# Optimization experiments

Hardware: AMD Instinct MI355X
Metric: run time of the kernel (lower is better)

## Reference

```python
import jax, jax.numpy as jnp
import numpy as np

INPUT_DIM, ATTN_DIM, OUTPUT_DIM = 1024, 1024, 1024
B, LQ, LKV = 4, 2048, 2048


def setup_inputs() -> dict:
    key = jax.random.key(0)
    ks = jax.random.split(key, 10)
    s = 1.0 / np.sqrt(INPUT_DIM)
    return {
        "primary": jax.random.normal(ks[0], (B, LQ, INPUT_DIM), jnp.float32),
        "context_sequence": jax.random.normal(ks[1], (B, LKV, INPUT_DIM), jnp.float32),
        "mask": jax.random.randint(ks[2], (B, LQ, LKV), 0, 2).astype(jnp.float32),
        "Wq": jax.random.uniform(ks[3], (INPUT_DIM, ATTN_DIM), jnp.float32, -s, s),
        "bq": jax.random.uniform(ks[4], (ATTN_DIM,), jnp.float32, -s, s),
        "Wk": jax.random.uniform(ks[5], (INPUT_DIM, ATTN_DIM), jnp.float32, -s, s),
        "bk": jax.random.uniform(ks[6], (ATTN_DIM,), jnp.float32, -s, s),
        "Wv": jax.random.uniform(ks[7], (INPUT_DIM, OUTPUT_DIM), jnp.float32, -s, s),
        "bv": jax.random.uniform(ks[8], (OUTPUT_DIM,), jnp.float32, -s, s),
    }


def reference(primary, context_sequence, mask, Wq, bq, Wk, bk, Wv, bv):
    q = primary @ Wq + bq                      # [B, Lq, attn_dim]
    k = context_sequence @ Wk + bk             # [B, Lkv, attn_dim]
    v = context_sequence @ Wv + bv             # [B, Lkv, output_dim]
    score = jnp.einsum('bqd,bkd->bqk', q, k) / jnp.sqrt(jnp.float32(ATTN_DIM))
    score = score + mask * (-1e9)
    attn = jax.nn.softmax(score, axis=-1)
    return jnp.einsum('bqk,bkd->bqd', attn, v)  # [B, Lq, output_dim]
```

## Files before the change

kernel.cpp:

```cpp
#include <hip/hip_runtime.h>
#include <stdint.h>

typedef unsigned short u16;
typedef unsigned char u8;
typedef __bf16 bf16_t;
typedef bf16_t bf16x8 __attribute__((ext_vector_type(8)));
typedef float f32x4 __attribute__((ext_vector_type(4)));
typedef u16 u16x4 __attribute__((ext_vector_type(4)));
typedef u16 u16x8 __attribute__((ext_vector_type(8)));

__device__ __forceinline__ u16 f2bf(float f) {
  union { float f; uint32_t u; } v;
  v.f = f;
  uint32_t u = v.u + 0x7fffu + ((v.u >> 16) & 1u);
  return (u16)(u >> 16);
}

__device__ __forceinline__ float bf2f(u16 x) {
  union { uint32_t u; float f; } v;
  v.u = ((uint32_t)x) << 16;
  return v.f;
}

__device__ __forceinline__ void gload16(const void* g, void* l) {
  __builtin_amdgcn_global_load_lds(
      (__attribute__((address_space(1))) void*)g,
      (__attribute__((address_space(3))) void*)l, 16, 0, 0);
}

__device__ __forceinline__ f32x4 mfma16(bf16x8 a, bf16x8 b, f32x4 c) {
  return __builtin_amdgcn_mfma_f32_16x16x32_bf16(a, b, c, 0, 0, 0);
}

__global__ __launch_bounds__(256) void cvt_wt(
    const float* __restrict__ prim, u16* __restrict__ prim_bf,
    const float* __restrict__ ctx, u16* __restrict__ ctx_bf,
    const float* __restrict__ Wq, const float* __restrict__ Wk,
    const float* __restrict__ Wv, u16* __restrict__ Oq,
    u16* __restrict__ Ok, u16* __restrict__ Ov) {
  int b = blockIdx.x;
  if (b < 2048) {
    const float* in = (b < 1024) ? prim : ctx;
    u16* out = (b < 1024) ? prim_bf : ctx_bf;
    int bb = b & 1023;
    int i = bb * 256 + threadIdx.x;
    const int n4 = 2097152;
    for (; i < n4; i += 1024 * 256) {
      float4 v = *((const float4*)in + i);
      u16x4 o;
      o.x = f2bf(v.x); o.y = f2bf(v.y); o.z = f2bf(v.z); o.w = f2bf(v.w);
      *((u16x4*)out + i) = o;
    }
  } else {
    int tb = b - 2048;
    int zi = tb >> 10, rem = tb & 1023;
    const float* W = zi == 0 ? Wq : (zi == 1 ? Wk : Wv);
    u16* O = zi == 0 ? Oq : (zi == 1 ? Ok : Ov);
    __shared__ float t[32][33];
    int x = threadIdx.x & 31, y = threadIdx.x >> 5;
    int n0 = (rem & 31) * 32, k0 = (rem >> 5) * 32;
#pragma unroll
    for (int i = 0; i < 32; i += 8)
      t[y + i][x] = W[(size_t)(k0 + y + i) * 1024 + n0 + x];
    __syncthreads();
#pragma unroll
    for (int i = 0; i < 32; i += 8)
      O[(size_t)(n0 + y + i) * 1024 + k0 + x] = f2bf(t[x][y + i]);
  }
}

template <typename CT>
__device__ __forceinline__ void gemm_body(
    u16* aL, u16* bL,
    const u16* __restrict__ A, const u16* __restrict__ Bt,
    const float* __restrict__ biasCol, const float* __restrict__ biasRow,
    CT* __restrict__ C, int bm, int bn, int K, int lda, int ldb, int ldc) {
  int tid = threadIdx.x;
  int lane = tid & 63, w = tid >> 6;
  int l15 = lane & 15, g = lane >> 4;
  int wr = w >> 2, wc = w & 3;
  int NT = K >> 6;

  f32x4 acc[8][4] = {};

  auto stageA = [&](int buf, int h, int tk) {
    int k0 = tk * 64;
    int r = tid >> 3, cd = (tid & 7) * 8;
    int cs = cd ^ ((r & 7) * 8);
    int row0 = h * 64 + r;
    gload16(A + (size_t)(bm + row0) * lda + k0 + cs, aL + buf * 16384 + row0 * 64 + cd);
    int row1 = row0 + 128;
    gload16(A + (size_t)(bm + row1) * lda + k0 + cs, aL + buf * 16384 + row1 * 64 + cd);
  };
  auto stageB = [&](int buf, int x, int tk) {
    int k0 = tk * 64;
#pragma unroll
    for (int l = 0; l < 2; ++l) {
      int u = l * 512 + tid;
      int r = u >> 3, cd = (u & 7) * 8;
      int cs = cd ^ ((r & 7) * 8);
      int row = x * 128 + r;
      gload16(Bt + (size_t)(bn + row) * ldb + k0 + cs, bL + buf * 16384 + row * 64 + cd);
    }
  };
  auto ldA = [&](int buf, int m, int kc) -> bf16x8 {
    int row = wr * 128 + m * 16 + l15;
    int col = (kc * 32 + g * 8) ^ ((row & 7) * 8);
    return *(const bf16x8*)(aL + buf * 16384 + row * 64 + col);
  };
  auto ldB = [&](int buf, int j, int kc) -> bf16x8 {
    int row = wc * 64 + j * 16 + l15;
    int col = (kc * 32 + g * 8) ^ ((row & 7) * 8);
    return *(const bf16x8*)(bL + buf * 16384 + row * 64 + col);
  };

  stageA(0, 0, 0);
  stageB(0, 0, 0);
  stageB(0, 1, 0);
  stageA(0, 1, 0);
  int t1c = NT > 1 ? 1 : 0;
  stageA(1, 0, t1c);
  stageB(1, 0, t1c);
  asm volatile("s_waitcnt vmcnt(6)" ::: "memory");
  __builtin_amdgcn_s_barrier();

  for (int t = 0; t < NT; ++t) {
    int cur = t & 1, nxt = cur ^ 1;
    int tn1 = (t + 1 < NT) ? t + 1 : NT - 1;
    int tn2 = (t + 2 < NT) ? t + 2 : NT - 1;
    bf16x8 a0[4], b0[4], b1[4];

#pragma unroll
    for (int i = 0; i < 4; ++i) a0[i] = ldA(cur, i, 0);
#pragma unroll
    for (int j = 0; j < 4; ++j) b0[j] = ldB(cur, j, 0);
    stageB(nxt, 1, tn1);
    __builtin_amdgcn_s_barrier();
    asm volatile("s_waitcnt lgkmcnt(0)" ::: "memory");
    __builtin_amdgcn_sched_barrier(0);
    __builtin_amdgcn_s_setprio(1);
#pragma unroll
    for (int i = 0; i < 4; ++i)
#pragma unroll
      for (int j = 0; j < 4; ++j) acc[i][j] = mfma16(a0[i], b0[j], acc[i][j]);
    __builtin_amdgcn_s_setprio(0);
    __builtin_amdgcn_s_barrier();

#pragma unroll
    for (int i = 0; i < 4; ++i) a0[i] = ldA(cur, i, 1);
#pragma unroll
    for (int j = 0; j < 4; ++j) b1[j] = ldB(cur, j, 1);
    stageA(nxt, 1, tn1);
    __builtin_amdgcn_s_barrier();
    asm volatile("s_waitcnt lgkmcnt(0)" ::: "memory");
    __builtin_amdgcn_sched_barrier(0);
    __builtin_amdgcn_s_setprio(1);
#pragma unroll
    for (int i = 0; i < 4; ++i)
#pragma unroll
      for (int j = 0; j < 4; ++j) acc[i][j] = mfma16(a0[i], b1[j], acc[i][j]);
    __builtin_amdgcn_s_setprio(0);
    asm volatile("s_waitcnt vmcnt(8)" ::: "memory");
    __builtin_amdgcn_s_barrier();

#pragma unroll
    for (int i = 0; i < 4; ++i) a0[i] = ldA(cur, 4 + i, 0);
    stageA(cur, 0, tn2);
    __builtin_amdgcn_s_barrier();
    asm volatile("s_waitcnt lgkmcnt(0)" ::: "memory");
    __builtin_amdgcn_sched_barrier(0);
    __builtin_amdgcn_s_setprio(1);
#pragma unroll
    for (int i = 0; i < 4; ++i)
#pragma unroll
      for (int j = 0; j < 4; ++j) acc[4 + i][j] = mfma16(a0[i], b0[j], acc[4 + i][j]);
    __builtin_amdgcn_s_setprio(0);
    __builtin_amdgcn_s_barrier();

#pragma unroll
    for (int i = 0; i < 4; ++i) a0[i] = ldA(cur, 4 + i, 1);
    stageB(cur, 0, tn2);
    __builtin_amdgcn_s_barrier();
    asm volatile("s_waitcnt lgkmcnt(0)" ::: "memory");
    __builtin_amdgcn_sched_barrier(0);
    __builtin_amdgcn_s_setprio(1);
#pragma unroll
    for (int i = 0; i < 4; ++i)
#pragma unroll
      for (int j = 0; j < 4; ++j) acc[4 + i][j] = mfma16(a0[i], b1[j], acc[4 + i][j]);
    __builtin_amdgcn_s_setprio(0);
    asm volatile("s_waitcnt vmcnt(6)" ::: "memory");
    __builtin_amdgcn_s_barrier();
  }

#pragma unroll
  for (int mi = 0; mi < 8; ++mi) {
    int row = bm + wr * 128 + mi * 16 + g * 4;
#pragma unroll
    for (int j = 0; j < 4; ++j) {
      int col = bn + wc * 64 + j * 16 + l15;
      float bcv = biasCol ? biasCol[col] : 0.0f;
#pragma unroll
      for (int rr = 0; rr < 4; ++rr) {
        float brv = biasRow ? biasRow[row + rr] : 0.0f;
        float v = acc[mi][j][rr] + bcv + brv;
        if constexpr (sizeof(CT) == 1) {
          unsigned int p = __builtin_amdgcn_cvt_pk_fp8_f32(v, v, 0, false);
          C[(size_t)(row + rr) * ldc + col] = (CT)(p & 0xff);
        } else if constexpr (sizeof(CT) == 2) {
          C[(size_t)(row + rr) * ldc + col] = f2bf(v);
        } else {
          C[(size_t)(row + rr) * ldc + col] = v;
        }
      }
    }
  }
}

__global__ __launch_bounds__(512, 2) void proj3(
    const u16* __restrict__ prim_ctx, const u16* __restrict__ wqk,
    const u16* __restrict__ wvt, const u16* __restrict__ ctx_bf,
    const float* __restrict__ bq, const float* __restrict__ bk,
    const float* __restrict__ bv,
    u8* __restrict__ qk8, u16* __restrict__ vt) {
  __shared__ u16 smem[4 * 16384];
  u16* aL = smem;
  u16* bL = smem + 2 * 16384;
  int bz = blockIdx.z;
  if (bz < 2) {
    gemm_body<u8>(aL, bL,
                  prim_ctx + (size_t)bz * 8192 * 1024,
                  wqk + (size_t)bz * 1024 * 1024,
                  bz ? bk : bq, nullptr,
                  qk8 + (size_t)bz * 8192 * 1024,
                  blockIdx.x * 256, blockIdx.y * 256, 1024, 1024, 1024, 1024);
  } else {
    int lin = blockIdx.x + 32 * blockIdx.y;
    gemm_body<u16>(aL, bL, wvt, ctx_bf, nullptr, bv, vt,
                   (lin & 3) * 256, (lin >> 2) * 256, 1024, 1024, 1024, 8192);
  }
}

__global__ __launch_bounds__(512, 2) void gemm_s8(
    const u8* __restrict__ A, const u8* __restrict__ Bt, u16* __restrict__ C) {
  const int lda = 1024, ldb = 1024, ldc = 2048, K = 1024;
  const u8* Ab = A + (size_t)blockIdx.z * 2048 * 1024;
  const u8* Bb = Bt + (size_t)blockIdx.z * 2048 * 1024;
  u16* Cb = C + (size_t)blockIdx.z * 2048 * 2048;
  int bm = blockIdx.x * 256, bn = blockIdx.y * 256;

  __shared__ u8 aLds[2][256 * 64];
  __shared__ u8 bLds[2][256 * 64];
  int tid = threadIdx.x;
  int lane = tid & 63, w = tid >> 6;
  int l15 = lane & 15, g = lane >> 4;
  int wr = w >> 2, wc = w & 3;
  int NT = K >> 6;

  f32x4 acc[8][4] = {};

  auto stageA = [&](int buf, int h, int tk) {
    int k0 = tk * 64;
    int r = tid >> 2;
    int row = h * 64 + (r & 63) + (r >> 6) * 128;
    int cd = (tid & 3) * 16;
    int cs = cd ^ ((row & 3) * 16);
    gload16(Ab + (size_t)(bm + row) * lda + k0 + cs, &aLds[buf][row * 64 + cd]);
  };
  auto stageB = [&](int buf, int x, int tk) {
    int k0 = tk * 64;
    int row = x * 128 + (tid >> 2);
    int cd = (tid & 3) * 16;
    int cs = cd ^ ((row & 3) * 16);
    gload16(Bb + (size_t)(bn + row) * ldb + k0 + cs, &bLds[buf][row * 64 + cd]);
  };
  auto ldA = [&](int buf, int m, int kc) -> long {
    int row = wr * 128 + m * 16 + l15;
    int colb = (kc * 32 + g * 8) ^ ((row & 3) * 16);
    return *(const long*)&aLds[buf][row * 64 + colb];
  };
  auto ldB = [&](int buf, int j, int kc) -> long {
    int row = wc * 64 + j * 16 + l15;
    int colb = (kc * 32 + g * 8) ^ ((row & 3) * 16);
    return *(const long*)&bLds[buf][row * 64 + colb];
  };

  stageA(0, 0, 0);
  stageB(0, 0, 0);
  stageB(0, 1, 0);
  stageA(0, 1, 0);
  int t1c = NT > 1 ? 1 : 0;
  stageA(1, 0, t1c);
  stageB(1, 0, t1c);
  asm volatile("s_waitcnt vmcnt(3)" ::: "memory");
  __builtin_amdgcn_s_barrier();

  for (int t = 0; t < NT; ++t) {
    int cur = t & 1, nxt = cur ^ 1;
    int tn1 = (t + 1 < NT) ? t + 1 : NT - 1;
    int tn2 = (t + 2 < NT) ? t + 2 : NT - 1;
    long a0[4], b0[4], b1[4];

#pragma unroll
    for (int i = 0; i < 4; ++i) a0[i] = ldA(cur, i, 0);
#pragma unroll
    for (int j = 0; j < 4; ++j) b0[j] = ldB(cur, j, 0);
    stageB(nxt, 1, tn1);
    __builtin_amdgcn_s_barrier();
    asm volatile("s_waitcnt lgkmcnt(0)" ::: "memory");
    __builtin_amdgcn_sched_barrier(0);
    __builtin_amdgcn_s_setprio(1);
#pragma unroll
    for (int i = 0; i < 4; ++i)
#pragma unroll
      for (int j = 0; j < 4; ++j)
        acc[i][j] = __builtin_amdgcn_mfma_f32_16x16x32_fp8_fp8(a0[i], b0[j], acc[i][j], 0, 0, 0);
    __builtin_amdgcn_s_setprio(0);
    __builtin_amdgcn_s_barrier();

#pragma unroll
    for (int i = 0; i < 4; ++i) a0[i] = ldA(cur, i, 1);
#pragma unroll
    for (int j = 0; j < 4; ++j) b1[j] = ldB(cur, j, 1);
    stageA(nxt, 1, tn1);
    __builtin_amdgcn_s_barrier();
    asm volatile("s_waitcnt lgkmcnt(0)" ::: "memory");
    __builtin_amdgcn_sched_barrier(0);
    __builtin_amdgcn_s_setprio(1);
#pragma unroll
    for (int i = 0; i < 4; ++i)
#pragma unroll
      for (int j = 0; j < 4; ++j)
        acc[i][j] = __builtin_amdgcn_mfma_f32_16x16x32_fp8_fp8(a0[i], b1[j], acc[i][j], 0, 0, 0);
    __builtin_amdgcn_s_setprio(0);
    asm volatile("s_waitcnt vmcnt(4)" ::: "memory");
    __builtin_amdgcn_s_barrier();

#pragma unroll
    for (int i = 0; i < 4; ++i) a0[i] = ldA(cur, 4 + i, 0);
    stageA(cur, 0, tn2);
    __builtin_amdgcn_s_barrier();
    asm volatile("s_waitcnt lgkmcnt(0)" ::: "memory");
    __builtin_amdgcn_sched_barrier(0);
    __builtin_amdgcn_s_setprio(1);
#pragma unroll
    for (int i = 0; i < 4; ++i)
#pragma unroll
      for (int j = 0; j < 4; ++j)
        acc[4 + i][j] = __builtin_amdgcn_mfma_f32_16x16x32_fp8_fp8(a0[i], b0[j], acc[4 + i][j], 0, 0, 0);
    __builtin_amdgcn_s_setprio(0);
    __builtin_amdgcn_s_barrier();

#pragma unroll
    for (int i = 0; i < 4; ++i) a0[i] = ldA(cur, 4 + i, 1);
    stageB(cur, 0, tn2);
    __builtin_amdgcn_s_barrier();
    asm volatile("s_waitcnt lgkmcnt(0)" ::: "memory");
    __builtin_amdgcn_sched_barrier(0);
    __builtin_amdgcn_s_setprio(1);
#pragma unroll
    for (int i = 0; i < 4; ++i)
#pragma unroll
      for (int j = 0; j < 4; ++j)
        acc[4 + i][j] = __builtin_amdgcn_mfma_f32_16x16x32_fp8_fp8(a0[i], b1[j], acc[4 + i][j], 0, 0, 0);
    __builtin_amdgcn_s_setprio(0);
    asm volatile("s_waitcnt vmcnt(3)" ::: "memory");
    __builtin_amdgcn_s_barrier();
  }

#pragma unroll
  for (int mi = 0; mi < 8; ++mi) {
    int row = bm + wr * 128 + mi * 16 + g * 4;
#pragma unroll
    for (int j = 0; j < 4; ++j) {
      int col = bn + wc * 64 + j * 16 + l15;
#pragma unroll
      for (int rr = 0; rr < 4; ++rr)
        Cb[(size_t)(row + rr) * ldc + col] = f2bf(acc[mi][j][rr]);
    }
  }
}

template <typename CT>
__global__ __launch_bounds__(512, 2) void gemm256(
    const u16* __restrict__ A, const u16* __restrict__ Bt,
    CT* __restrict__ C, int K, int lda, int ldb, int ldc,
    long long bsA, long long bsB, long long bsC) {
  __shared__ u16 smem[4 * 16384];
  gemm_body<CT>(smem, smem + 2 * 16384,
                A + (size_t)blockIdx.z * bsA, Bt + (size_t)blockIdx.z * bsB,
                nullptr, nullptr, C + (size_t)blockIdx.z * bsC,
                blockIdx.x * 256, blockIdx.y * 256, K, lda, ldb, ldc);
}

__global__ __launch_bounds__(256) void softmax_mask(
    const u16* __restrict__ S, const float* __restrict__ mask, u16* __restrict__ P) {
  const float C1 = 0.04508422f;
  const float C2 = -1.4426950e9f;
  int wid = (blockIdx.x * blockDim.x + threadIdx.x) >> 6;
  int lane = threadIdx.x & 63;
  size_t base = (size_t)wid * 2048;
  const u16* sp = S + base;
  const float* mp = mask + base;

  float a[32];
#pragma unroll
  for (int pass = 0; pass < 4; ++pass) {
    int e0 = pass * 512 + lane * 8;
    u16x8 sv = *(const u16x8*)(sp + e0);
    float4 m0 = *(const float4*)(mp + e0);
    float4 m1 = *(const float4*)(mp + e0 + 4);
    a[pass * 8 + 0] = bf2f(sv[0]) * C1 + m0.x * C2;
    a[pass * 8 + 1] = bf2f(sv[1]) * C1 + m0.y * C2;
    a[pass * 8 + 2] = bf2f(sv[2]) * C1 + m0.z * C2;
    a[pass * 8 + 3] = bf2f(sv[3]) * C1 + m0.w * C2;
    a[pass * 8 + 4] = bf2f(sv[4]) * C1 + m1.x * C2;
    a[pass * 8 + 5] = bf2f(sv[5]) * C1 + m1.y * C2;
    a[pass * 8 + 6] = bf2f(sv[6]) * C1 + m1.z * C2;
    a[pass * 8 + 7] = bf2f(sv[7]) * C1 + m1.w * C2;
  }
  float m = a[0];
#pragma unroll
  for (int i = 1; i < 32; ++i) m = fmaxf(m, a[i]);
#pragma unroll
  for (int off = 32; off >= 1; off >>= 1) m = fmaxf(m, __shfl_xor(m, off));

  float s = 0.0f;
#pragma unroll
  for (int i = 0; i < 32; ++i) {
    a[i] = exp2f(a[i] - m);
    s += a[i];
  }
#pragma unroll
  for (int off = 32; off >= 1; off >>= 1) s += __shfl_xor(s, off);
  float inv = 1.0f / s;

  u16* pp = P + base;
#pragma unroll
  for (int pass = 0; pass < 4; ++pass) {
    int e0 = pass * 512 + lane * 8;
    u16x8 o;
#pragma unroll
    for (int j = 0; j < 8; ++j) o[j] = f2bf(a[pass * 8 + j] * inv);
    *(u16x8*)(pp + e0) = o;
  }
}

extern "C" void kernel_launch(void* const* d_in, const int* in_sizes, int n_in,
                              void* d_out, int out_size, void* d_ws, size_t ws_size,
                              hipStream_t stream) {
  const float* primary = (const float*)d_in[0];
  const float* ctx     = (const float*)d_in[1];
  const float* mask    = (const float*)d_in[2];
  const float* Wq      = (const float*)d_in[3];
  const float* bq      = (const float*)d_in[4];
  const float* Wk      = (const float*)d_in[5];
  const float* bk      = (const float*)d_in[6];
  const float* Wv      = (const float*)d_in[7];
  const float* bv      = (const float*)d_in[8];
  float* out = (float*)d_out;

  char* ws = (char*)d_ws;
  u8*  qk8     = (u8*)(ws);
  u16* vtbf    = (u16*)(ws + 2 * 16777216);
  u16* prim_bf = (u16*)(ws + 3 * 16777216);
  u16* ctx_bf  = (u16*)(ws + 4 * 16777216);
  u16* wqt     = (u16*)(ws + 5 * 16777216);
  u16* wkt     = (u16*)(ws + 5 * 16777216 + 2097152);
  u16* wvt     = (u16*)(ws + 5 * 16777216 + 2 * 2097152);
  u16* sbf     = (u16*)(ws + 3 * 16777216);
  u16* pbf     = (u16*)(ws);

  cvt_wt<<<5120, 256, 0, stream>>>(primary, prim_bf, ctx, ctx_bf,
                                   Wq, Wk, Wv, wqt, wkt, wvt);
  proj3<<<dim3(32, 4, 3), 512, 0, stream>>>(
      prim_bf, wqt, wvt, ctx_bf, bq, bk, bv, qk8, vtbf);
  gemm_s8<<<dim3(8, 8, 4), 512, 0, stream>>>(qk8, qk8 + 8192 * 1024, sbf);
  softmax_mask<<<2048, 256, 0, stream>>>(sbf, mask, pbf);
  gemm256<float><<<dim3(8, 4, 4), 512, 0, stream>>>(
      pbf, vtbf, out, 2048, 2048, 8192, 1024,
      2048 * 2048LL, 2048LL, 2048 * 1024LL);
}
```

Before: 219.8 us.

## Restructure bf16 GEMM mainloop into 4-stage K32 pipeline with one barrier

New measurement: 225.6 us. +2.6%, slower.

```diff
diff --git a/kernel.cpp b/kernel.cpp
--- a/kernel.cpp
+++ b/kernel.cpp
@@ -79,117 +79,69 @@
   int lane = tid & 63, w = tid >> 6;
   int l15 = lane & 15, g = lane >> 4;
   int wr = w >> 2, wc = w & 3;
-  int NT = K >> 6;
+  int NT = K >> 5;
 
   f32x4 acc[8][4] = {};
 
-  auto stageA = [&](int buf, int h, int tk) {
-    int k0 = tk * 64;
-    int r = tid >> 3, cd = (tid & 7) * 8;
-    int cs = cd ^ ((r & 7) * 8);
-    int row0 = h * 64 + r;
-    gload16(A + (size_t)(bm + row0) * lda + k0 + cs, aL + buf * 16384 + row0 * 64 + cd);
-    int row1 = row0 + 128;
-    gload16(A + (size_t)(bm + row1) * lda + k0 + cs, aL + buf * 16384 + row1 * 64 + cd);
-  };
-  auto stageB = [&](int buf, int x, int tk) {
-    int k0 = tk * 64;
+  auto stageA = [&](int buf, int tk) {
+    int k0 = tk * 32;
 #pragma unroll
     for (int l = 0; l < 2; ++l) {
       int u = l * 512 + tid;
-      int r = u >> 3, cd = (u & 7) * 8;
-      int cs = cd ^ ((r & 7) * 8);
-      int row = x * 128 + r;
-      gload16(Bt + (size_t)(bn + row) * ldb + k0 + cs, bL + buf * 16384 + row * 64 + cd);
+      int row = u >> 2;
+      int slot = (u & 3) ^ ((row >> 2) & 3);
+      gload16(A + (size_t)(bm + row) * lda + k0 + slot * 8,
+              aL + buf * 8192 + row * 32 + (u & 3) * 8);
     }
   };
-  auto ldA = [&](int buf, int m, int kc) -> bf16x8 {
+  auto stageB = [&](int buf, int tk) {
+    int k0 = tk * 32;
+#pragma unroll
+    for (int l = 0; l < 2; ++l) {
+      int u = l * 512 + tid;
+      int row = u >> 2;
+      int slot = (u & 3) ^ ((row >> 2) & 3);
+      gload16(Bt + (size_t)(bn + row) * ldb + k0 + slot * 8,
+              bL + buf * 8192 + row * 32 + (u & 3) * 8);
+    }
+  };
+  auto ldA = [&](int buf, int m) -> bf16x8 {
     int row = wr * 128 + m * 16 + l15;
-    int col = (kc * 32 + g * 8) ^ ((row & 7) * 8);
-    return *(const bf16x8*)(aL + buf * 16384 + row * 64 + col);
-  };
-  auto ldB = [&](int buf, int j, int kc) -> bf16x8 {
+    int col = (g ^ ((row >> 2) & 3)) * 8;
+    return *(const bf16x8*)(aL + buf * 8192 + row * 32 + col);
+  };
+  auto ldB = [&](int buf, int j) -> bf16x8 {
     int row = wc * 64 + j * 16 + l15;
-    int col = (kc * 32 + g * 8) ^ ((row & 7) * 8);
-    return *(const bf16x8*)(bL + buf * 16384 + row * 64 + col);
-  };
-
-  stageA(0, 0, 0);
-  stageB(0, 0, 0);
-  stageB(0, 1, 0);
-  stageA(0, 1, 0);
-  int t1c = NT > 1 ? 1 : 0;
-  stageA(1, 0, t1c);
-  stageB(1, 0, t1c);
-  asm volatile("s_waitcnt vmcnt(6)" ::: "memory");
+    int col = (g ^ ((row >> 2) & 3)) * 8;
+    return *(const bf16x8*)(bL + buf * 8192 + row * 32 + col);
+  };
+
+  stageA(0, 0); stageB(0, 0);
+  stageA(1, NT > 1 ? 1 : 0); stageB(1, NT > 1 ? 1 : 0);
+  stageA(2, NT > 2 ? 2 : 0); stageB(2, NT > 2 ? 2 : 0);
+  asm volatile("s_waitcnt vmcnt(8)" ::: "memory");
   __builtin_amdgcn_s_barrier();
 
   for (int t = 0; t < NT; ++t) {
-    int cur = t & 1, nxt = cur ^ 1;
-    int tn1 = (t + 1 < NT) ? t + 1 : NT - 1;
-    int tn2 = (t + 2 < NT) ? t + 2 : NT - 1;
-    bf16x8 a0[4], b0[4], b1[4];
-
-#pragma unroll
-    for (int i = 0; i < 4; ++i) a0[i] = ldA(cur, i, 0);
-#pragma unroll
-    for (int j = 0; j < 4; ++j) b0[j] = ldB(cur, j, 0);
-    stageB(nxt, 1, tn1);
-    __builtin_amdgcn_s_barrier();
+    int buf = t & 3;
+    int tn3 = (t + 3 < NT) ? t + 3 : NT - 1;
+    int bn3 = (t + 3) & 3;
+    bf16x8 af[8], bfv[4];
+#pragma unroll
+    for (int m = 0; m < 8; ++m) af[m] = ldA(buf, m);
+#pragma unroll
+    for (int j = 0; j < 4; ++j) bfv[j] = ldB(buf, j);
+    stageA(bn3, tn3);
+    stageB(bn3, tn3);
     asm volatile("s_waitcnt lgkmcnt(0)" ::: "memory");
     __builtin_amdgcn_sched_barrier(0);
     __builtin_amdgcn_s_setprio(1);
 #pragma unroll
-    for (int i = 0; i < 4; ++i)
-#pragma unroll
-      for (int j = 0; j < 4; ++j) acc[i][j] = mfma16(a0[i], b0[j], acc[i][j]);
-    __builtin_amdgcn_s_setprio(0);
-    __builtin_amdgcn_s_barrier();
-
-#pragma unroll
-    for (int i = 0; i < 4; ++i) a0[i] = ldA(cur, i, 1);
-#pragma unroll
-    for (int j = 0; j < 4; ++j) b1[j] = ldB(cur, j, 1);
-    stageA(nxt, 1, tn1);
-    __builtin_amdgcn_s_barrier();
-    asm volatile("s_waitcnt lgkmcnt(0)" ::: "memory");
-    __builtin_amdgcn_sched_barrier(0);
-    __builtin_amdgcn_s_setprio(1);
-#pragma unroll
-    for (int i = 0; i < 4; ++i)
-#pragma unroll
-      for (int j = 0; j < 4; ++j) acc[i][j] = mfma16(a0[i], b1[j], acc[i][j]);
+    for (int m = 0; m < 8; ++m)
+#pragma unroll
+      for (int j = 0; j < 4; ++j) acc[m][j] = mfma16(af[m], bfv[j], acc[m][j]);
     __builtin_amdgcn_s_setprio(0);
     asm volatile("s_waitcnt vmcnt(8)" ::: "memory");
-    __builtin_amdgcn_s_barrier();
-
-#pragma unroll
-    for (int i = 0; i < 4; ++i) a0[i] = ldA(cur, 4 + i, 0);
-    stageA(cur, 0, tn2);
-    __builtin_amdgcn_s_barrier();
-    asm volatile("s_waitcnt lgkmcnt(0)" ::: "memory");
-    __builtin_amdgcn_sched_barrier(0);
-    __builtin_amdgcn_s_setprio(1);
-#pragma unroll
-    for (int i = 0; i < 4; ++i)
-#pragma unroll
-      for (int j = 0; j < 4; ++j) acc[4 + i][j] = mfma16(a0[i], b0[j], acc[4 + i][j]);
-    __builtin_amdgcn_s_setprio(0);
-    __builtin_amdgcn_s_barrier();
-
-#pragma unroll
-    for (int i = 0; i < 4; ++i) a0[i] = ldA(cur, 4 + i, 1);
-    stageB(cur, 0, tn2);
-    __builtin_amdgcn_s_barrier();
-    asm volatile("s_waitcnt lgkmcnt(0)" ::: "memory");
-    __builtin_amdgcn_sched_barrier(0);
-    __builtin_amdgcn_s_setprio(1);
-#pragma unroll
-    for (int i = 0; i < 4; ++i)
-#pragma unroll
-      for (int j = 0; j < 4; ++j) acc[4 + i][j] = mfma16(a0[i], b1[j], acc[4 + i][j]);
-    __builtin_amdgcn_s_setprio(0);
-    asm volatile("s_waitcnt vmcnt(6)" ::: "memory");
     __builtin_amdgcn_s_barrier();
   }
 
@@ -223,9 +175,9 @@
     const float* __restrict__ bq, const float* __restrict__ bk,
     const float* __restrict__ bv,
     u8* __restrict__ qk8, u16* __restrict__ vt) {
-  __shared__ u16 smem[4 * 16384];
+  __shared__ u16 smem[2 * 4 * 8192];
   u16* aL = smem;
-  u16* bL = smem + 2 * 16384;
+  u16* bL = smem + 4 * 8192;
   int bz = blockIdx.z;
   if (bz < 2) {
     gemm_body<u8>(aL, bL,
@@ -386,8 +338,8 @@
     const u16* __restrict__ A, const u16* __restrict__ Bt,
     CT* __restrict__ C, int K, int lda, int ldb, int ldc,
     long long bsA, long long bsB, long long bsC) {
-  __shared__ u16 smem[4 * 16384];
-  gemm_body<CT>(smem, smem + 2 * 16384,
+  __shared__ u16 smem[2 * 4 * 8192];
+  gemm_body<CT>(smem, smem + 4 * 8192,
                 A + (size_t)blockIdx.z * bsA, Bt + (size_t)blockIdx.z * bsB,
                 nullptr, nullptr, C + (size_t)blockIdx.z * bsC,
                 blockIdx.x * 256, blockIdx.y * 256, K, lda, ldb, ldc);
```

## Move V projection into softmax kernel and run softmax in place

Applied to the files above, without the earlier changes.

Result: faster. 206.8 us (-5.9%).

```diff
diff --git a/kernel.cpp b/kernel.cpp
--- a/kernel.cpp
+++ b/kernel.cpp
@@ -217,36 +217,29 @@
   }
 }
 
-__global__ __launch_bounds__(512, 2) void proj3(
+__global__ __launch_bounds__(512, 2) void proj_qk(
     const u16* __restrict__ prim_ctx, const u16* __restrict__ wqk,
-    const u16* __restrict__ wvt, const u16* __restrict__ ctx_bf,
     const float* __restrict__ bq, const float* __restrict__ bk,
-    const float* __restrict__ bv,
-    u8* __restrict__ qk8, u16* __restrict__ vt) {
+    u8* __restrict__ qk8) {
   __shared__ u16 smem[4 * 16384];
-  u16* aL = smem;
-  u16* bL = smem + 2 * 16384;
   int bz = blockIdx.z;
-  if (bz < 2) {
-    gemm_body<u8>(aL, bL,
-                  prim_ctx + (size_t)bz * 8192 * 1024,
-                  wqk + (size_t)bz * 1024 * 1024,
-                  bz ? bk : bq, nullptr,
-                  qk8 + (size_t)bz * 8192 * 1024,
-                  blockIdx.x * 256, blockIdx.y * 256, 1024, 1024, 1024, 1024);
-  } else {
-    int lin = blockIdx.x + 32 * blockIdx.y;
-    gemm_body<u16>(aL, bL, wvt, ctx_bf, nullptr, bv, vt,
-                   (lin & 3) * 256, (lin >> 2) * 256, 1024, 1024, 1024, 8192);
-  }
+  gemm_body<u8>(smem, smem + 2 * 16384,
+                prim_ctx + (size_t)bz * 8192 * 1024,
+                wqk + (size_t)bz * 1024 * 1024,
+                bz ? bk : bq, nullptr,
+                qk8 + (size_t)bz * 8192 * 1024,
+                blockIdx.x * 256, blockIdx.y * 256, 1024, 1024, 1024, 1024);
 }
 
 __global__ __launch_bounds__(512, 2) void gemm_s8(
-    const u8* __restrict__ A, const u8* __restrict__ Bt, u16* __restrict__ C) {
+    const u8* __restrict__ A, const u8* __restrict__ Bt,
+    u16* __restrict__ Clo, u16* __restrict__ Chi) {
   const int lda = 1024, ldb = 1024, ldc = 2048, K = 1024;
-  const u8* Ab = A + (size_t)blockIdx.z * 2048 * 1024;
-  const u8* Bb = Bt + (size_t)blockIdx.z * 2048 * 1024;
-  u16* Cb = C + (size_t)blockIdx.z * 2048 * 2048;
+  int bz = blockIdx.z;
+  const u8* Ab = A + (size_t)bz * 2048 * 1024;
+  const u8* Bb = Bt + (size_t)bz * 2048 * 1024;
+  u16* Cb = (bz < 2) ? Clo + (size_t)bz * 2048 * 2048
+                     : Chi + (size_t)(bz - 2) * 2048 * 2048;
   int bm = blockIdx.x * 256, bn = blockIdx.y * 256;
 
   __shared__ u8 aLds[2][256 * 64];
@@ -381,27 +374,25 @@
   }
 }
 
-template <typename CT>
-__global__ __launch_bounds__(512, 2) void gemm256(
-    const u16* __restrict__ A, const u16* __restrict__ Bt,
-    CT* __restrict__ C, int K, int lda, int ldb, int ldc,
-    long long bsA, long long bsB, long long bsC) {
+__global__ __launch_bounds__(512, 2) void vt_softmax(
+    const u16* __restrict__ wvt, const u16* __restrict__ ctx_bf,
+    const float* __restrict__ bv, u16* __restrict__ vt,
+    u16* __restrict__ Slo, u16* __restrict__ Shi,
+    const float* __restrict__ mask) {
   __shared__ u16 smem[4 * 16384];
-  gemm_body<CT>(smem, smem + 2 * 16384,
-                A + (size_t)blockIdx.z * bsA, Bt + (size_t)blockIdx.z * bsB,
-                nullptr, nullptr, C + (size_t)blockIdx.z * bsC,
-                blockIdx.x * 256, blockIdx.y * 256, K, lda, ldb, ldc);
-}
-
-__global__ __launch_bounds__(256) void softmax_mask(
-    const u16* __restrict__ S, const float* __restrict__ mask, u16* __restrict__ P) {
+  int b = blockIdx.x;
+  if (b < 128) {
+    gemm_body<u16>(smem, smem + 2 * 16384, wvt, ctx_bf, nullptr, bv, vt,
+                   (b & 3) * 256, (b >> 2) * 256, 1024, 1024, 1024, 8192);
+    return;
+  }
   const float C1 = 0.04508422f;
   const float C2 = -1.4426950e9f;
-  int wid = (blockIdx.x * blockDim.x + threadIdx.x) >> 6;
+  int row = (b - 128) * 8 + (threadIdx.x >> 6);
   int lane = threadIdx.x & 63;
-  size_t base = (size_t)wid * 2048;
-  const u16* sp = S + base;
-  const float* mp = mask + base;
+  u16* sp = (row < 4096) ? Slo + (size_t)row * 2048
+                         : Shi + (size_t)(row - 4096) * 2048;
+  const float* mp = mask + (size_t)row * 2048;
 
   float a[32];
 #pragma unroll
@@ -435,15 +426,26 @@
   for (int off = 32; off >= 1; off >>= 1) s += __shfl_xor(s, off);
   float inv = 1.0f / s;
 
-  u16* pp = P + base;
 #pragma unroll
   for (int pass = 0; pass < 4; ++pass) {
     int e0 = pass * 512 + lane * 8;
     u16x8 o;
 #pragma unroll
     for (int j = 0; j < 8; ++j) o[j] = f2bf(a[pass * 8 + j] * inv);
-    *(u16x8*)(pp + e0) = o;
-  }
+    *(u16x8*)(sp + e0) = o;
+  }
+}
+
+__global__ __launch_bounds__(512, 2) void gemm_pv(
+    const u16* __restrict__ Alo, const u16* __restrict__ Ahi,
+    const u16* __restrict__ Bt, float* __restrict__ C) {
+  __shared__ u16 smem[4 * 16384];
+  int bz = blockIdx.z;
+  const u16* A = (bz < 2) ? Alo + (size_t)bz * 2048 * 2048
+                          : Ahi + (size_t)(bz - 2) * 2048 * 2048;
+  gemm_body<float>(smem, smem + 2 * 16384, A, Bt + (size_t)bz * 2048,
+                   nullptr, nullptr, C + (size_t)bz * 2048 * 1024,
+                   blockIdx.x * 256, blockIdx.y * 256, 2048, 2048, 8192, 1024);
 }
 
 extern "C" void kernel_launch(void* const* d_in, const int* in_sizes, int n_in,
@@ -461,23 +463,22 @@
   float* out = (float*)d_out;
 
   char* ws = (char*)d_ws;
-  u8*  qk8     = (u8*)(ws);
-  u16* vtbf    = (u16*)(ws + 2 * 16777216);
-  u16* prim_bf = (u16*)(ws + 3 * 16777216);
-  u16* ctx_bf  = (u16*)(ws + 4 * 16777216);
+  u16* prim_bf = (u16*)(ws);
+  u16* ctx_bf  = (u16*)(ws + 16777216);
+  u8*  qk8     = (u8*)(ws + 2 * 16777216);
+  u16* vtbf    = (u16*)(ws + 3 * 16777216);
+  u16* sbf_lo  = (u16*)(ws);
+  u16* sbf_hi  = (u16*)(ws + 4 * 16777216);
   u16* wqt     = (u16*)(ws + 5 * 16777216);
   u16* wkt     = (u16*)(ws + 5 * 16777216 + 2097152);
   u16* wvt     = (u16*)(ws + 5 * 16777216 + 2 * 2097152);
-  u16* sbf     = (u16*)(ws + 3 * 16777216);
-  u16* pbf     = (u16*)(ws);
 
   cvt_wt<<<5120, 256, 0, stream>>>(primary, prim_bf, ctx, ctx_bf,
                                    Wq, Wk, Wv, wqt, wkt, wvt);
-  proj3<<<dim3(32, 4, 3), 512, 0, stream>>>(
-      prim_bf, wqt, wvt, ctx_bf, bq, bk, bv, qk8, vtbf);
-  gemm_s8<<<dim3(8, 8, 4), 512, 0, stream>>>(qk8, qk8 + 8192 * 1024, sbf);
-  softmax_mask<<<2048, 256, 0, stream>>>(sbf, mask, pbf);
-  gemm256<float><<<dim3(8, 4, 4), 512, 0, stream>>>(
-      pbf, vtbf, out, 2048, 2048, 8192, 1024,
-      2048 * 2048LL, 2048LL, 2048 * 1024LL);
-}
+  proj_qk<<<dim3(32, 4, 2), 512, 0, stream>>>(prim_bf, wqt, bq, bk, qk8);
+  gemm_s8<<<dim3(8, 8, 4), 512, 0, stream>>>(qk8, qk8 + 8192 * 1024,
+                                             sbf_lo, sbf_hi);
+  vt_softmax<<<1152, 512, 0, stream>>>(wvt, ctx_bf, bv, vtbf,
+                                       sbf_lo, sbf_hi, mask);
+  gemm_pv<<<dim3(8, 4, 4), 512, 0, stream>>>(sbf_lo, sbf_hi, vtbf, out);
+}
```
